# Kernel optimization log

Measured on AMD Instinct MI355X. Metric: run time of the kernel, lower is better.

The kernel has to match this reference:

```python
import jax, jax.numpy as jnp
import numpy as np

WINDOW = 32
CHUNK = 16


def _z_indices(size: int) -> np.ndarray:
    # Faithful port of VisualRetina._precompute_z (Morton/Z-order permutation).
    y = np.repeat(np.arange(size), size)
    x = np.tile(np.arange(size), size)
    z = np.zeros_like(y)
    for i in range(8):
        z |= ((x & (1 << i)) << i) | ((y & (1 << i)) << (i + 1))
    # z values are unique for size<=256, so argsort order is unambiguous
    return np.argsort(z)


def setup_inputs() -> dict:
    key = jax.random.key(0)
    x = jax.random.normal(key, (256, 3, 224, 224), dtype=jnp.float32)
    return {"x": x}


def reference(x):
    B, C, H, W = x.shape
    ws = WINDOW
    # F.interpolate default mode='nearest': src_idx = floor(dst_idx * in/out)
    ih = (jnp.arange(ws) * H) // ws
    iw = (jnp.arange(ws) * W) // ws
    x_resized = x[:, :, ih, :][:, :, :, iw]              # [B,C,32,32]

    zi = jnp.asarray(_z_indices(ws))                      # [1024] fixed permutation
    x_flat = x_resized.reshape(B, C, ws * ws)
    x_z = x_flat[:, :, zi]                                # Z-order gather

    num_chunks = (ws * ws) // CHUNK                       # 64
    chunks = x_z.reshape(B, C, num_chunks, CHUNK)

    t = jnp.linspace(-1.0, 1.0, CHUNK)
    T_mat = jnp.stack([t ** 3, t ** 2, t, jnp.ones_like(t)], axis=1)  # [16,4]
    T_pinv = jnp.linalg.pinv(T_mat)                       # [4,16]

    y = jnp.transpose(chunks, (0, 2, 3, 1))               # [B,nc,16,C]
    coeffs = jnp.einsum('kt,bntc->bnkc', T_pinv, y)       # [B,nc,4,C]
    y_pred = jnp.einsum('tk,bnkc->bntc', T_mat, coeffs)   # [B,nc,16,C]

    residuals = jnp.mean((y - y_pred) ** 2, axis=2)       # [B,nc,C]
    sigma = jnp.sqrt(residuals)[:, :, None, :]            # [B,nc,1,C]

    token_data = jnp.concatenate([coeffs, sigma], axis=2) # [B,nc,5,C]
    structure = token_data.mean(axis=-1)                  # [B,nc,5]
    return structure[:, :, None, :]                       # [B,nc,1,5]
```

## Files before the change

kernel.cpp:

```cpp
#include <hip/hip_runtime.h>


#define BATCH 256
#define NCHUNK 64
#define HW 224

__global__ __launch_bounds__(64) void retina_kernel(const float* __restrict__ x,
                                                    float* __restrict__ out) {
    int tid = blockIdx.x * blockDim.x + threadIdx.x;
    if (tid >= BATCH * NCHUNK) return;
    int b = tid >> 6;
    int n = tid & 63;
    int xh = (n & 1) | ((n >> 1) & 2) | ((n >> 2) & 4);
    int yh = ((n >> 1) & 1) | ((n >> 2) & 2) | ((n >> 3) & 4);
    const float* __restrict__ xb = x + (size_t)b * 3 * HW * HW;

    float s0[3] = {0.f, 0.f, 0.f};
    float s1[3] = {0.f, 0.f, 0.f};
    float s2[3] = {0.f, 0.f, 0.f};
    float s3[3] = {0.f, 0.f, 0.f};
    float sq[3] = {0.f, 0.f, 0.f};

#pragma unroll
    for (int t = 0; t < 16; ++t) {
        int dx = (t & 1) | ((t >> 1) & 2);
        int dy = ((t >> 1) & 1) | ((t >> 2) & 2);
        int h = 7 * (4 * yh + dy);
        int w = 7 * (4 * xh + dx);
        int off = h * HW + w;
        float tt = -1.0f + (2.0f / 15.0f) * (float)t;
        float t2 = tt * tt;
        float t3 = t2 * tt;
#pragma unroll
        for (int c = 0; c < 3; ++c) {
            float v = xb[c * (HW * HW) + off];
            s0[c] += v;
            s1[c] += tt * v;
            s2[c] += t2 * v;
            s3[c] += t3 * v;
            sq[c] += v * v;
        }
    }

    const float S0f = 16.0f;
    const float S2f = 1360.0f / 225.0f;
    const float S4f = 206992.0f / 50625.0f;
    const float S6f = 37308880.0f / 11390625.0f;
    const float inv_det_odd  = 1.0f / (S6f * S2f - S4f * S4f);
    const float inv_det_even = 1.0f / (S4f * S0f - S2f * S2f);

    float m0 = 0.f, m1 = 0.f, m2 = 0.f, m3 = 0.f, ms = 0.f;
#pragma unroll
    for (int c = 0; c < 3; ++c) {
        float a_cube = (S2f * s3[c] - S4f * s1[c]) * inv_det_odd;
        float a_lin  = (S6f * s1[c] - S4f * s3[c]) * inv_det_odd;
        float a_quad = (S0f * s2[c] - S2f * s0[c]) * inv_det_even;
        float a_cons = (S4f * s0[c] - S2f * s2[c]) * inv_det_even;
        float ss = sq[c] - (a_cube * s3[c] + a_quad * s2[c] +
                            a_lin * s1[c] + a_cons * s0[c]);
        float sig = sqrtf(fmaxf(ss, 0.0f) * (1.0f / 16.0f));
        m0 += a_cube; m1 += a_quad; m2 += a_lin; m3 += a_cons; ms += sig;
    }

    float* o = out + (size_t)tid * 5;
    const float third = 1.0f / 3.0f;
    o[0] = m0 * third;
    o[1] = m1 * third;
    o[2] = m2 * third;
    o[3] = m3 * third;
    o[4] = ms * third;
}

extern "C" void kernel_launch(void* const* d_in, const int* in_sizes, int n_in,
                              void* d_out, int out_size, void* d_ws, size_t ws_size,
                              hipStream_t stream) {
    const float* x = (const float*)d_in[0];
    float* out = (float*)d_out;
    int total = BATCH * NCHUNK;
    int block = 64;
    int grid = (total + block - 1) / block;
    retina_kernel<<<grid, block, 0, stream>>>(x, out);
}
```

Baseline: 183.7 us.

## Stage strided pixel gather in shared memory with row-contiguous loads per channel

Each block now handles one batch image with 192 threads, one group of 64 per channel. The groups cooperatively load the 32x32 nearest-neighbour samples into shared memory in row-major order, so neighbouring lanes read pixels along the same row. After a barrier, 64 threads compute the per-chunk cubic fit from shared memory. This is meant to replace the scattered Z-order global reads with better-grouped ones and issue more loads in parallel. In exchange, two thirds of the threads sit idle during the fit phase and a block-wide synchronisation is added.

```diff
diff --git a/kernel.cpp b/kernel.cpp
--- a/kernel.cpp
+++ b/kernel.cpp
@@ -5,70 +5,84 @@
 #define NCHUNK 64
 #define HW 224
 
-__global__ __launch_bounds__(64) void retina_kernel(const float* __restrict__ x,
-                                                    float* __restrict__ out) {
-    int tid = blockIdx.x * blockDim.x + threadIdx.x;
-    if (tid >= BATCH * NCHUNK) return;
-    int b = tid >> 6;
-    int n = tid & 63;
-    int xh = (n & 1) | ((n >> 1) & 2) | ((n >> 2) & 4);
-    int yh = ((n >> 1) & 1) | ((n >> 2) & 2) | ((n >> 3) & 4);
-    const float* __restrict__ xb = x + (size_t)b * 3 * HW * HW;
+__global__ __launch_bounds__(192) void retina_kernel(const float* __restrict__ x,
+                                                     float* __restrict__ out) {
+    __shared__ float g[3][1024];
 
-    float s0[3] = {0.f, 0.f, 0.f};
-    float s1[3] = {0.f, 0.f, 0.f};
-    float s2[3] = {0.f, 0.f, 0.f};
-    float s3[3] = {0.f, 0.f, 0.f};
-    float sq[3] = {0.f, 0.f, 0.f};
+    int b = blockIdx.x;
+    int j = threadIdx.x;
+    int c = j >> 6;
+    int l = j & 63;
+
+    const float* __restrict__ xc = x + ((size_t)b * 3 + c) * (HW * HW);
 
 #pragma unroll
-    for (int t = 0; t < 16; ++t) {
-        int dx = (t & 1) | ((t >> 1) & 2);
-        int dy = ((t >> 1) & 1) | ((t >> 2) & 2);
-        int h = 7 * (4 * yh + dy);
-        int w = 7 * (4 * xh + dx);
-        int off = h * HW + w;
-        float tt = -1.0f + (2.0f / 15.0f) * (float)t;
-        float t2 = tt * tt;
-        float t3 = t2 * tt;
+    for (int i = 0; i < 16; ++i) {
+        int e = (i << 6) + l;
+        int y = e >> 5;
+        int xg = e & 31;
+        g[c][e] = xc[(7 * y) * HW + 7 * xg];
+    }
+    __syncthreads();
+
+    if (j < 64) {
+        int n = j;
+        int xh = (n & 1) | ((n >> 1) & 2) | ((n >> 2) & 4);
+        int yh = ((n >> 1) & 1) | ((n >> 2) & 2) | ((n >> 3) & 4);
+
+        float s0[3] = {0.f, 0.f, 0.f};
+        float s1[3] = {0.f, 0.f, 0.f};
+        float s2[3] = {0.f, 0.f, 0.f};
+        float s3[3] = {0.f, 0.f, 0.f};
+        float sq[3] = {0.f, 0.f, 0.f};
+
 #pragma unroll
-        for (int c = 0; c < 3; ++c) {
-            float v = xb[c * (HW * HW) + off];
-            s0[c] += v;
-            s1[c] += tt * v;
-            s2[c] += t2 * v;
-            s3[c] += t3 * v;
-            sq[c] += v * v;
+        for (int t = 0; t < 16; ++t) {
+            int dx = (t & 1) | ((t >> 1) & 2);
+            int dy = ((t >> 1) & 1) | ((t >> 2) & 2);
+            int idx = (4 * yh + dy) * 32 + (4 * xh + dx);
+            float tt = -1.0f + (2.0f / 15.0f) * (float)t;
+            float t2 = tt * tt;
+            float t3 = t2 * tt;
+#pragma unroll
+            for (int cc = 0; cc < 3; ++cc) {
+                float v = g[cc][idx];
+                s0[cc] += v;
+                s1[cc] += tt * v;
+                s2[cc] += t2 * v;
+                s3[cc] += t3 * v;
+                sq[cc] += v * v;
+            }
         }
+
+        const float S0f = 16.0f;
+        const float S2f = 1360.0f / 225.0f;
+        const float S4f = 206992.0f / 50625.0f;
+        const float S6f = 37308880.0f / 11390625.0f;
+        const float inv_det_odd  = 1.0f / (S6f * S2f - S4f * S4f);
+        const float inv_det_even = 1.0f / (S4f * S0f - S2f * S2f);
+
+        float m0 = 0.f, m1 = 0.f, m2 = 0.f, m3 = 0.f, ms = 0.f;
+#pragma unroll
+        for (int cc = 0; cc < 3; ++cc) {
+            float a_cube = (S2f * s3[cc] - S4f * s1[cc]) * inv_det_odd;
+            float a_lin  = (S6f * s1[cc] - S4f * s3[cc]) * inv_det_odd;
+            float a_quad = (S0f * s2[cc] - S2f * s0[cc]) * inv_det_even;
+            float a_cons = (S4f * s0[cc] - S2f * s2[cc]) * inv_det_even;
+            float ss = sq[cc] - (a_cube * s3[cc] + a_quad * s2[cc] +
+                                 a_lin * s1[cc] + a_cons * s0[cc]);
+            float sig = sqrtf(fmaxf(ss, 0.0f) * (1.0f / 16.0f));
+            m0 += a_cube; m1 += a_quad; m2 += a_lin; m3 += a_cons; ms += sig;
+        }
+
+        float* o = out + ((size_t)b * NCHUNK + n) * 5;
+        const float third = 1.0f / 3.0f;
+        o[0] = m0 * third;
+        o[1] = m1 * third;
+        o[2] = m2 * third;
+        o[3] = m3 * third;
+        o[4] = ms * third;
     }
-
-    const float S0f = 16.0f;
-    const float S2f = 1360.0f / 225.0f;
-    const float S4f = 206992.0f / 50625.0f;
-    const float S6f = 37308880.0f / 11390625.0f;
-    const float inv_det_odd  = 1.0f / (S6f * S2f - S4f * S4f);
-    const float inv_det_even = 1.0f / (S4f * S0f - S2f * S2f);
-
-    float m0 = 0.f, m1 = 0.f, m2 = 0.f, m3 = 0.f, ms = 0.f;
-#pragma unroll
-    for (int c = 0; c < 3; ++c) {
-        float a_cube = (S2f * s3[c] - S4f * s1[c]) * inv_det_odd;
-        float a_lin  = (S6f * s1[c] - S4f * s3[c]) * inv_det_odd;
-        float a_quad = (S0f * s2[c] - S2f * s0[c]) * inv_det_even;
-        float a_cons = (S4f * s0[c] - S2f * s2[c]) * inv_det_even;
-        float ss = sq[c] - (a_cube * s3[c] + a_quad * s2[c] +
-                            a_lin * s1[c] + a_cons * s0[c]);
-        float sig = sqrtf(fmaxf(ss, 0.0f) * (1.0f / 16.0f));
-        m0 += a_cube; m1 += a_quad; m2 += a_lin; m3 += a_cons; ms += sig;
-    }
-
-    float* o = out + (size_t)tid * 5;
-    const float third = 1.0f / 3.0f;
-    o[0] = m0 * third;
-    o[1] = m1 * third;
-    o[2] = m2 * third;
-    o[3] = m3 * third;
-    o[4] = ms * third;
 }
 
 extern "C" void kernel_launch(void* const* d_in, const int* in_sizes, int n_in,
@@ -76,8 +90,5 @@
                               hipStream_t stream) {
     const float* x = (const float*)d_in[0];
     float* out = (float*)d_out;
-    int total = BATCH * NCHUNK;
-    int block = 64;
-    int grid = (total + block - 1) / block;
-    retina_kernel<<<grid, block, 0, stream>>>(x, out);
+    retina_kernel<<<BATCH, 192, 0, stream>>>(x, out);
 }
```

Measured after the change: 184.9 us. Within noise of the previous version (+0.7%).
